# Performance work log

Measured on AMD Instinct MI355X. Metric: run time of the kernel, lower is better.

The kernel has to match this reference:

```python
import jax, jax.numpy as jnp
import numpy as np

NUM_EXPERTS = 64
TOTAL_TOKENS = 67108864  # 64M-entry dispatch buffer
MAX_COUNT = 2 * TOTAL_TOKENS // NUM_EXPERTS  # E[sum(counts)] ~ TOTAL_TOKENS


def setup_inputs() -> dict:
    key = jax.random.key(0)
    k1, = jax.random.split(key, 1)
    num_recv_tokens_per_expert = jax.random.randint(
        k1, (NUM_EXPERTS,), 0, MAX_COUNT, dtype=jnp.int32)
    expert_start_loc = jnp.zeros((NUM_EXPERTS,), dtype=jnp.int32)
    m_indices = jnp.zeros((TOTAL_TOKENS,), dtype=jnp.int32)
    return {
        "num_recv_tokens_per_expert": num_recv_tokens_per_expert,
        "expert_start_loc": expert_start_loc,
        "m_indices": m_indices,
    }


def reference(num_recv_tokens_per_expert, expert_start_loc, m_indices):
    counts = num_recv_tokens_per_expert
    # exclusive cumsum -> per-expert start offsets (written to expert_start_loc)
    starts = (jnp.cumsum(counts) - counts).astype(jnp.int32)
    total = starts[-1] + counts[-1]  # total dispatched tokens
    idx = jnp.arange(m_indices.shape[0], dtype=jnp.int32)
    # token i belongs to the LAST expert whose start <= i (matches the torch
    # loop's overwrite order for zero-count experts): searchsorted-right - 1.
    expert_ids = (jnp.searchsorted(starts, idx, side='right') - 1).astype(jnp.int32)
    # positions beyond the total token count are never written by the loop.
    m_out = jnp.where(idx < total, expert_ids, m_indices)
    return m_out, starts
```

## Files before the change

kernel.cpp:

```cpp
#include <hip/hip_runtime.h>


#define N_EXPERTS 64
#define BLOCK 256
#define V4_PER_THREAD 4
#define ELEMS_PER_BLOCK (BLOCK * 4 * V4_PER_THREAD)

__global__ void moe_scan_kernel(const int* __restrict__ counts,
                                int* __restrict__ starts_out,
                                int* __restrict__ ws) {
    int lane = threadIdx.x;
    int c = counts[lane];
    int x = c;
#pragma unroll
    for (int off = 1; off < 64; off <<= 1) {
        int y = __shfl_up(x, off, 64);
        if (lane >= off) x += y;
    }
    int start = x - c;
    starts_out[lane] = start;
    ws[lane] = start;
    if (lane == 63) ws[64] = x;
}

__device__ __forceinline__ int upper_bound_m1(const int* __restrict__ s, int i) {
    int e = 0;
#pragma unroll
    for (int step = 32; step >= 1; step >>= 1) {
        if (s[e + step] <= i) e += step;
    }
    return e;
}

__global__ __launch_bounds__(BLOCK) void moe_fill_kernel(
    const int* __restrict__ ws,
    const int* __restrict__ m_in,
    int* __restrict__ m_out,
    int n) {
    __shared__ int s_starts[N_EXPERTS];
    __shared__ int s_total_sh;
    int tid = threadIdx.x;
    if (tid < N_EXPERTS) s_starts[tid] = ws[tid];
    if (tid == 0) s_total_sh = ws[N_EXPERTS];
    __syncthreads();

    int total = s_total_sh;
    if (total > n) total = n;
    if (total < 0) total = 0;

    int blockBase = blockIdx.x * ELEMS_PER_BLOCK;
#pragma unroll
    for (int v = 0; v < V4_PER_THREAD; ++v) {
        int i0 = blockBase + (v * BLOCK + tid) * 4;
        if (i0 >= n) break;
        int4 outv;
        if (i0 + 3 < total) {
            int e0 = upper_bound_m1(s_starts, i0);
            int e3 = upper_bound_m1(s_starts, i0 + 3);
            if (e0 == e3) {
                outv.x = e0; outv.y = e0; outv.z = e0; outv.w = e0;
            } else {
                outv.x = e0;
                outv.y = upper_bound_m1(s_starts, i0 + 1);
                outv.z = upper_bound_m1(s_starts, i0 + 2);
                outv.w = e3;
            }
        } else if (i0 >= total) {
            outv = *reinterpret_cast<const int4*>(m_in + i0);
        } else {
            int vals[4];
#pragma unroll
            for (int j = 0; j < 4; ++j) {
                int i = i0 + j;
                vals[j] = (i < total) ? upper_bound_m1(s_starts, i) : m_in[i];
            }
            outv.x = vals[0]; outv.y = vals[1]; outv.z = vals[2]; outv.w = vals[3];
        }
        *reinterpret_cast<int4*>(m_out + i0) = outv;
    }
}

extern "C" void kernel_launch(void* const* d_in, const int* in_sizes, int n_in,
                              void* d_out, int out_size, void* d_ws, size_t ws_size,
                              hipStream_t stream) {
    const int* counts = (const int*)d_in[0];
    const int* m_in = (const int*)d_in[2];
    int n = in_sizes[2];
    int* out = (int*)d_out;
    int* starts_out = out + n;
    int* ws = (int*)d_ws;

    moe_scan_kernel<<<1, 64, 0, stream>>>(counts, starts_out, ws);

    int blocks = (n + ELEMS_PER_BLOCK - 1) / ELEMS_PER_BLOCK;
    moe_fill_kernel<<<blocks, BLOCK, 0, stream>>>(ws, m_in, out, n);
}
```

Measured before the change: 380.6 us.

## Fuse expert-offset scan into fill kernel and add block-uniform fast paths

Removes the separate single-wave scan kernel: every block now recomputes the 64-entry exclusive prefix sum with wave shuffles into shared memory, and block 0 writes the starts output. This drops one kernel launch and the dependency through the workspace. It also adds block-level fast paths: if a whole block maps to one expert it stores a constant vector without per-element searches, and if a block lies entirely past the total it does a plain copy. The cost is that every block redundantly loads the counts and runs the scan.

```diff
diff --git a/kernel.cpp b/kernel.cpp
--- a/kernel.cpp
+++ b/kernel.cpp
@@ -5,23 +5,6 @@
 #define BLOCK 256
 #define V4_PER_THREAD 4
 #define ELEMS_PER_BLOCK (BLOCK * 4 * V4_PER_THREAD)
-
-__global__ void moe_scan_kernel(const int* __restrict__ counts,
-                                int* __restrict__ starts_out,
-                                int* __restrict__ ws) {
-    int lane = threadIdx.x;
-    int c = counts[lane];
-    int x = c;
-#pragma unroll
-    for (int off = 1; off < 64; off <<= 1) {
-        int y = __shfl_up(x, off, 64);
-        if (lane >= off) x += y;
-    }
-    int start = x - c;
-    starts_out[lane] = start;
-    ws[lane] = start;
-    if (lane == 63) ws[64] = x;
-}
 
 __device__ __forceinline__ int upper_bound_m1(const int* __restrict__ s, int i) {
     int e = 0;
@@ -32,23 +15,61 @@
     return e;
 }
 
-__global__ __launch_bounds__(BLOCK) void moe_fill_kernel(
-    const int* __restrict__ ws,
+__global__ __launch_bounds__(BLOCK) void moe_fused_kernel(
+    const int* __restrict__ counts,
     const int* __restrict__ m_in,
     int* __restrict__ m_out,
+    int* __restrict__ starts_out,
     int n) {
-    __shared__ int s_starts[N_EXPERTS];
-    __shared__ int s_total_sh;
+    __shared__ int s_starts[N_EXPERTS + 1];
     int tid = threadIdx.x;
-    if (tid < N_EXPERTS) s_starts[tid] = ws[tid];
-    if (tid == 0) s_total_sh = ws[N_EXPERTS];
+
+    if (tid < 64) {
+        int c = counts[tid];
+        int x = c;
+#pragma unroll
+        for (int off = 1; off < 64; off <<= 1) {
+            int y = __shfl_up(x, off, 64);
+            if (tid >= off) x += y;
+        }
+        s_starts[tid] = x - c;
+        if (tid == 63) s_starts[64] = x;
+        if (blockIdx.x == 0) starts_out[tid] = x - c;
+    }
     __syncthreads();
 
-    int total = s_total_sh;
+    int total = s_starts[64];
     if (total > n) total = n;
     if (total < 0) total = 0;
 
     int blockBase = blockIdx.x * ELEMS_PER_BLOCK;
+    if (blockBase >= n) return;
+    int blockEnd = blockBase + ELEMS_PER_BLOCK;
+    bool fullBlock = (blockEnd <= n);
+    if (!fullBlock) blockEnd = n;
+
+    if (fullBlock && blockEnd <= total) {
+        int eA = upper_bound_m1(s_starts, blockBase);
+        int eB = upper_bound_m1(s_starts, blockEnd - 1);
+        if (eA == eB) {
+            int4 val; val.x = eA; val.y = eA; val.z = eA; val.w = eA;
+#pragma unroll
+            for (int v = 0; v < V4_PER_THREAD; ++v) {
+                int i0 = blockBase + (v * BLOCK + tid) * 4;
+                *reinterpret_cast<int4*>(m_out + i0) = val;
+            }
+            return;
+        }
+    } else if (fullBlock && blockBase >= total) {
+#pragma unroll
+        for (int v = 0; v < V4_PER_THREAD; ++v) {
+            int i0 = blockBase + (v * BLOCK + tid) * 4;
+            *reinterpret_cast<int4*>(m_out + i0) =
+                *reinterpret_cast<const int4*>(m_in + i0);
+        }
+        return;
+    }
+
 #pragma unroll
     for (int v = 0; v < V4_PER_THREAD; ++v) {
         int i0 = blockBase + (v * BLOCK + tid) * 4;
@@ -88,10 +109,7 @@
     int n = in_sizes[2];
     int* out = (int*)d_out;
     int* starts_out = out + n;
-    int* ws = (int*)d_ws;
-
-    moe_scan_kernel<<<1, 64, 0, stream>>>(counts, starts_out, ws);
 
     int blocks = (n + ELEMS_PER_BLOCK - 1) / ELEMS_PER_BLOCK;
-    moe_fill_kernel<<<blocks, BLOCK, 0, stream>>>(ws, m_in, out, n);
+    moe_fused_kernel<<<blocks, BLOCK, 0, stream>>>(counts, m_in, out, starts_out, n);
 }
```

Measured after the change: 378.3 us. Within noise of the previous version (-0.6%).
